# Kernel tuning notes

Hardware: AMD Instinct MI355X
Metric: run time of the kernel (lower is better)

## Reference

```python
import jax, jax.numpy as jnp
import numpy as np

B, NUM_FRAMES, NUM_PATCHES = 2, 16, 196
DIM, H, DH = 768, 12, 64
T = NUM_FRAMES * NUM_PATCHES  # 3136
EPS = 1e-5


def setup_inputs() -> dict:
    key = jax.random.key(0)
    ks = jax.random.split(key, 5)
    x = jax.random.normal(ks[0], (B, T, DIM), jnp.float32)
    context = jax.random.normal(ks[1], (B, T, DIM), jnp.float32)
    Wq = jax.random.normal(ks[2], (DIM, H * DH), jnp.float32) * 0.02
    Wkv = jax.random.normal(ks[3], (DIM, 2 * H * DH), jnp.float32) * 0.02
    Wo = jax.random.normal(ks[4], (H * DH, DIM), jnp.float32) * 0.02
    bo = jnp.zeros((DIM,), jnp.float32)
    gamma = jnp.ones((DIM,), jnp.float32)
    beta = jnp.zeros((DIM,), jnp.float32)
    # block-diagonal frame mask: patch i attends to patch j iff same frame
    frame_ids = jnp.arange(T) // NUM_PATCHES
    mask = frame_ids[:, None] == frame_ids[None, :]  # [T, T] bool
    return {"x": x, "context": context, "Wq": Wq, "Wkv": Wkv, "Wo": Wo,
            "bo": bo, "gamma": gamma, "beta": beta, "mask": mask}


def reference(x, context, Wq, Wkv, Wo, bo, gamma, beta, mask):
    # LayerNorm on queries only (torch LN: biased variance, eps=1e-5)
    mu = jnp.mean(x, axis=-1, keepdims=True)
    var = jnp.var(x, axis=-1, keepdims=True)
    xn = (x - mu) * jax.lax.rsqrt(var + EPS) * gamma + beta

    q = xn @ Wq                      # [B, T, H*DH]
    kv = context @ Wkv               # [B, T, 2*H*DH]
    k, v = jnp.split(kv, 2, axis=-1)

    def split_heads(t):
        return t.reshape(B, T, H, DH).transpose(0, 2, 1, 3)  # [B, H, T, DH]

    q, k, v = split_heads(q), split_heads(k), split_heads(v)

    scale = DH ** -0.5
    dots = jnp.einsum('bhnd,bhmd->bhnm', q, k) * scale      # [B, H, T, T]
    dots = jnp.where(mask, dots, -jnp.inf)
    attn = jax.nn.softmax(dots, axis=-1)                    # dropout p=0.0 -> identity
    out = jnp.einsum('bhnm,bhmd->bhnd', attn, v)            # [B, H, T, DH]
    out = out.transpose(0, 2, 1, 3).reshape(B, T, H * DH)
    return out @ Wo + bo
```

## Files before the change

kernel.cpp:

```cpp
#include <hip/hip_runtime.h>
#include <hip/hip_bf16.h>

#define NB 2
#define TT 3136
#define DIM 768
#define NH 12
#define NF 16
#define NP 196

typedef __attribute__((ext_vector_type(8))) short short8;
typedef __attribute__((ext_vector_type(4))) short s16x4;
typedef __attribute__((ext_vector_type(4))) float f32x4;
typedef unsigned int uint;

__device__ __forceinline__ float bf2f(short s) {
    return __uint_as_float(((uint)(unsigned short)s) << 16);
}
__device__ __forceinline__ short f2bs(float f) {
    __hip_bfloat16 h = __float2bfloat16(f);
    short s; __builtin_memcpy(&s, &h, 2); return s;
}
__device__ __forceinline__ uint pack2bf(float a, float b) {
    return (uint)(unsigned short)f2bs(a) | ((uint)(unsigned short)f2bs(b) << 16);
}
__device__ __forceinline__ void load16_lds(const void* g, void* l) {
    __builtin_amdgcn_global_load_lds(
        (const __attribute__((address_space(1))) unsigned int*)g,
        (__attribute__((address_space(3))) unsigned int*)l, 16, 0, 0);
}

__global__ __launch_bounds__(256)
void prep_all(const float* __restrict__ Wq, const float* __restrict__ Wkv,
              const float* __restrict__ Wo,
              __hip_bfloat16* __restrict__ WqT, __hip_bfloat16* __restrict__ WkvT,
              __hip_bfloat16* __restrict__ WoT,
              const float* __restrict__ ctx, __hip_bfloat16* __restrict__ cb,
              const float* __restrict__ x, const float* __restrict__ gamma,
              const float* __restrict__ beta, __hip_bfloat16* __restrict__ xn) {
    __shared__ float tile[32][33];
    int blk = blockIdx.x, tid = threadIdx.x;
    if (blk < 2304) {
        int bx = blk % 96, ky = blk / 96;
        const float* W; __hip_bfloat16* WT; int N, n0;
        if (bx < 24)      { W = Wq;  WT = WqT;  N = DIM;     n0 = bx * 32; }
        else if (bx < 72) { W = Wkv; WT = WkvT; N = 2 * DIM; n0 = (bx - 24) * 32; }
        else              { W = Wo;  WT = WoT;  N = DIM;     n0 = (bx - 72) * 32; }
        int k0 = ky * 32;
        int tx = tid & 31, ty = tid >> 5;
#pragma unroll
        for (int i = 0; i < 32; i += 8)
            tile[ty + i][tx] = W[(size_t)(k0 + ty + i) * N + (n0 + tx)];
        __syncthreads();
#pragma unroll
        for (int i = 0; i < 32; i += 8)
            WT[(size_t)(n0 + ty + i) * DIM + (k0 + tx)] = __float2bfloat16(tile[tx][ty + i]);
        return;
    }
    blk -= 2304;
    if (blk < 4704) {
        size_t i = (size_t)blk * 256 + tid;
        f32x4 f; __builtin_memcpy(&f, ctx + i * 4, 16);
        s16x4 s;
#pragma unroll
        for (int j = 0; j < 4; j++) s[j] = f2bs(f[j]);
        __builtin_memcpy((short*)cb + i * 4, &s, 8);
        return;
    }
    blk -= 4704;
    int wave = tid >> 6, lane = tid & 63;
    int row = blk * 4 + wave;
    const float* xr = x + (size_t)row * DIM;
    f32x4 v[3];
    float s = 0.f, ss = 0.f;
#pragma unroll
    for (int i = 0; i < 3; i++) {
        __builtin_memcpy(&v[i], xr + lane * 4 + i * 256, 16);
#pragma unroll
        for (int j = 0; j < 4; j++) { s += v[i][j]; ss += v[i][j] * v[i][j]; }
    }
#pragma unroll
    for (int off = 32; off; off >>= 1) {
        s += __shfl_xor(s, off);
        ss += __shfl_xor(ss, off);
    }
    float mu = s / DIM;
    float rs = rsqrtf(ss / DIM - mu * mu + 1e-5f);
#pragma unroll
    for (int i = 0; i < 3; i++) {
        int c = lane * 4 + i * 256;
        f32x4 g, bt;
        __builtin_memcpy(&g, gamma + c, 16);
        __builtin_memcpy(&bt, beta + c, 16);
        s16x4 o;
#pragma unroll
        for (int j = 0; j < 4; j++) o[j] = f2bs((v[i][j] - mu) * rs * g[j] + bt[j]);
        __builtin_memcpy((short*)xn + (size_t)row * DIM + c, &o, 8);
    }
}

__global__ __launch_bounds__(512, 1)
void gemm_qkv(const __hip_bfloat16* __restrict__ xn,
              const __hip_bfloat16* __restrict__ cb,
              const __hip_bfloat16* __restrict__ WqT,
              const __hip_bfloat16* __restrict__ WkvT,
              __hip_bfloat16* __restrict__ qbuf,
              __hip_bfloat16* __restrict__ kvbuf) {
    __shared__ short lds[2][2][2][8192];

    int orig = blockIdx.x;
    int xcd = orig & 7, pos = orig >> 3;
    int wgid = (xcd < 1 ? xcd * 29 : 29 + (xcd - 1) * 28) + pos;
    int mt = wgid / 9, nt = wgid - mt * 9;

    const __hip_bfloat16 *Abase, *Bbase; __hip_bfloat16* Cbase;
    int N, n0;
    if (nt < 3) { Abase = xn; Bbase = WqT;  Cbase = qbuf;  N = DIM;  n0 = nt * 256; }
    else        { Abase = cb; Bbase = WkvT; Cbase = kvbuf; N = 1536; n0 = (nt - 3) * 256; }
    int m0 = mt * 256;

    int tid = threadIdx.x, lane = tid & 63, wave = tid >> 6;
    int r = lane & 15, q = lane >> 4;
    int wm = wave >> 2, wn = wave & 3;
    f32x4 acc[8][4] = {};

    auto stageK = [&](int buf, int kt) {
        int k0 = kt * 64;
#pragma unroll
        for (int h = 0; h < 2; h++)
#pragma unroll
            for (int s = 0; s < 2; s++) {
                int idx = s * 512 + tid;
                int row = idx >> 3, cg = idx & 7;
                int w = (cg << 4) ^ ((row & 7) << 4);
                int grow = m0 + h * 128 + row;
                if (grow > TT * NB - 1) grow = TT * NB - 1;
                load16_lds((const char*)Abase + ((size_t)grow * DIM + k0) * 2 + w,
                           (char*)&lds[buf][0][h][0] + idx * 16);
            }
#pragma unroll
        for (int h = 0; h < 2; h++)
#pragma unroll
            for (int s = 0; s < 2; s++) {
                int idx = s * 512 + tid;
                int row = idx >> 3, cg = idx & 7;
                int w = (cg << 4) ^ ((row & 7) << 4);
                int grow = n0 + h * 128 + row;
                load16_lds((const char*)Bbase + ((size_t)grow * DIM + k0) * 2 + w,
                           (char*)&lds[buf][1][h][0] + idx * 16);
            }
    };

    auto read_frag = [&](const char* base, int frag, int ks) {
        short8 v;
        int row_ = frag * 16 + r;
        int byte_ = row_ * 128 + ((ks * 64 + q * 16) ^ ((r & 7) << 4));
        __builtin_memcpy(&v, base + byte_, 16);
        return v;
    };

    stageK(0, 0);
    asm volatile("s_waitcnt vmcnt(0)" ::: "memory");
    __builtin_amdgcn_s_barrier();

    for (int t = 0; t < 12; ++t) {
        int cur = t & 1;
        const char* Ah = (const char*)&lds[cur][0][wm][0];
        const char* Bh = (const char*)&lds[cur][1][wn >> 1][0];
        int bbase = (wn & 1) * 4;
        short8 breg[4][2];
#pragma unroll
        for (int p = 0; p < 4; p++) {
            short8 areg[2][2];
#pragma unroll
            for (int i = 0; i < 2; i++)
#pragma unroll
                for (int ks = 0; ks < 2; ks++)
                    areg[i][ks] = read_frag(Ah, p * 2 + i, ks);
            if (p == 0) {
#pragma unroll
                for (int n = 0; n < 4; n++)
#pragma unroll
                    for (int ks = 0; ks < 2; ks++)
                        breg[n][ks] = read_frag(Bh, bbase + n, ks);
                if (t < 11) stageK(cur ^ 1, t + 1);
            }
            __builtin_amdgcn_s_barrier();
            __builtin_amdgcn_s_setprio(1);
#pragma unroll
            for (int i = 0; i < 2; i++)
#pragma unroll
                for (int n = 0; n < 4; n++)
#pragma unroll
                    for (int ks = 0; ks < 2; ks++)
                        acc[p * 2 + i][n] = __builtin_amdgcn_mfma_f32_16x16x32_bf16(
                            areg[i][ks], breg[n][ks], acc[p * 2 + i][n], 0, 0, 0);
            __builtin_amdgcn_s_setprio(0);
            if (p == 3)
                asm volatile("s_waitcnt vmcnt(0)" ::: "memory");
            __builtin_amdgcn_s_barrier();
        }
    }

#pragma unroll
    for (int mf = 0; mf < 8; mf++)
#pragma unroll
        for (int n = 0; n < 4; n++)
#pragma unroll
            for (int rr = 0; rr < 4; rr++) {
                int row = m0 + wm * 128 + mf * 16 + q * 4 + rr;
                if (row < TT * NB) {
                    int col = n0 + wn * 64 + n * 16 + r;
                    Cbase[(size_t)row * N + col] = __float2bfloat16(acc[mf][n][rr]);
                }
            }
}

__global__ __launch_bounds__(256)
void gemm_o(const __hip_bfloat16* __restrict__ A,
            const __hip_bfloat16* __restrict__ BT,
            const float* __restrict__ bias,
            float* __restrict__ C) {
    __shared__ short sA[2][128 * 64];
    __shared__ short sB[2][128 * 64];
    int orig = blockIdx.x;
    int xcd = orig & 7, pos = orig >> 3;
    int wgid = (xcd < 6 ? xcd * 37 : 222 + (xcd - 6) * 36) + pos;
    int mt = wgid / 6, nt = wgid - mt * 6;
    int m0 = mt * 128, n0 = nt * 128;
    int tid = threadIdx.x, lane = tid & 63, wave = tid >> 6;
    int r = lane & 15, q = lane >> 4;
    int wm = (wave & 1) * 64, wn = (wave >> 1) * 64;
    f32x4 acc[4][4] = {};

    auto stage = [&](int buf, int k0) {
#pragma unroll
        for (int i = 0; i < 4; i++) {
            int c = i * 256 + tid;
            int row = c >> 3, cg = c & 7;
            load16_lds(A + (size_t)(m0 + row) * DIM + k0 + cg * 8, &sA[buf][c * 8]);
        }
#pragma unroll
        for (int i = 0; i < 4; i++) {
            int c = i * 256 + tid;
            int row = c >> 3, cg = c & 7;
            load16_lds(BT + (size_t)(n0 + row) * DIM + k0 + cg * 8, &sB[buf][c * 8]);
        }
    };
    auto compute = [&](int buf) {
#pragma unroll
        for (int ks = 0; ks < 2; ks++) {
            short8 af[4], bfv[4];
#pragma unroll
            for (int t = 0; t < 4; t++) {
                __builtin_memcpy(&af[t],  &sA[buf][(wm + t * 16 + r) * 64 + ks * 32 + q * 8], 16);
                __builtin_memcpy(&bfv[t], &sB[buf][(wn + t * 16 + r) * 64 + ks * 32 + q * 8], 16);
            }
            __builtin_amdgcn_s_setprio(1);
#pragma unroll
            for (int mi = 0; mi < 4; mi++)
#pragma unroll
                for (int ni = 0; ni < 4; ni++)
                    acc[mi][ni] = __builtin_amdgcn_mfma_f32_16x16x32_bf16(
                        af[mi], bfv[ni], acc[mi][ni], 0, 0, 0);
            __builtin_amdgcn_s_setprio(0);
        }
    };

    stage(0, 0);
    __syncthreads();
    int cur = 0;
#pragma unroll 2
    for (int t = 0; t < 11; ++t) {
        stage(cur ^ 1, (t + 1) * 64);
        compute(cur);
        __syncthreads();
        cur ^= 1;
    }
    compute(cur);

    float bv[4];
#pragma unroll
    for (int ni = 0; ni < 4; ni++) bv[ni] = bias[n0 + wn + ni * 16 + r];
#pragma unroll
    for (int mi = 0; mi < 4; mi++)
#pragma unroll
        for (int ni = 0; ni < 4; ni++)
#pragma unroll
            for (int rr = 0; rr < 4; rr++) {
                int row = m0 + wm + mi * 16 + q * 4 + rr;
                int col = n0 + wn + ni * 16 + r;
                C[(size_t)row * DIM + col] = acc[mi][ni][rr] + bv[ni];
            }
}

__global__ __launch_bounds__(448, 4)
void attn_kernel(__hip_bfloat16* qo,
                 const __hip_bfloat16* __restrict__ kvb) {
    __shared__ short sK[208 * 66];
    __shared__ short sVT[64 * 226];
    int blk = blockIdx.x;
    int f = blk % NF, h = (blk / NF) % NH, b = blk / (NF * NH);
    size_t tok0 = (size_t)b * TT + (size_t)f * NP;
    int tid = threadIdx.x, wave = tid >> 6, lane = tid & 63;
    int r = lane & 15, q = lane >> 4;

    short8 qf[2][2];
#pragma unroll
    for (int half = 0; half < 2; half++) {
        int qrow = half * 98 + wave * 16 + r;
        if (qrow >= NP) qrow = 0;
        const __hip_bfloat16* src = qo + (tok0 + qrow) * DIM + h * 64;
        __builtin_memcpy(&qf[half][0], src + q * 8, 16);
        __builtin_memcpy(&qf[half][1], src + 32 + q * 8, 16);
    }

    for (int e = tid; e < 1664; e += 448) {
        int row = e >> 3, cg = e & 7;
        short8 t = {0,0,0,0,0,0,0,0};
        if (row < NP)
            __builtin_memcpy(&t, kvb + (tok0 + row) * 1536 + h * 64 + cg * 8, 16);
        __builtin_memcpy(&sK[row * 66 + cg * 8], &t, 16);
    }
    for (int jj = 0; jj < 224; jj += 28) {
        int j = jj + (tid >> 4);
        int d = (tid & 15) * 4;
        s16x4 v = {0, 0, 0, 0};
        if (j < NP)
            __builtin_memcpy(&v, kvb + (tok0 + j) * 1536 + DIM + h * 64 + d, 8);
#pragma unroll
        for (int i = 0; i < 4; i++) sVT[(d + i) * 226 + j] = v[i];
    }
    __syncthreads();

#pragma unroll
    for (int half = 0; half < 2; half++) {
        int row0 = half * 98;

        f32x4 sacc[13];
#pragma unroll
        for (int jf = 0; jf < 13; jf++) {
            f32x4 a = {};
            short8 kf;
            __builtin_memcpy(&kf, &sK[(jf * 16 + r) * 66 + q * 8], 16);
            a = __builtin_amdgcn_mfma_f32_16x16x32_bf16(kf, qf[half][0], a, 0, 0, 0);
            __builtin_memcpy(&kf, &sK[(jf * 16 + r) * 66 + 32 + q * 8], 16);
            a = __builtin_amdgcn_mfma_f32_16x16x32_bf16(kf, qf[half][1], a, 0, 0, 0);
            sacc[jf] = a;
        }

        const float scale = 0.125f;
        float mx = -INFINITY;
#pragma unroll
        for (int jf = 0; jf < 13; jf++)
#pragma unroll
            for (int rg = 0; rg < 4; rg++) {
                bool valid = (jf < 12) | (q == 0);
                if (valid) mx = fmaxf(mx, sacc[jf][rg] * scale);
            }
        mx = fmaxf(mx, __shfl_xor(mx, 16));
        mx = fmaxf(mx, __shfl_xor(mx, 32));
        float ps = 0.f;
#pragma unroll
        for (int jf = 0; jf < 13; jf++)
#pragma unroll
            for (int rg = 0; rg < 4; rg++) {
                bool valid = (jf < 12) | (q == 0);
                float p = valid ? __expf(sacc[jf][rg] * scale - mx) : 0.f;
                sacc[jf][rg] = p;
                ps += p;
            }
        ps += __shfl_xor(ps, 16);
        ps += __shfl_xor(ps, 32);
        float inv = 1.f / ps;

        uint pk01[13], pk23[13];
#pragma unroll
        for (int jf = 0; jf < 13; jf++) {
            pk01[jf] = pack2bf(sacc[jf][0] * inv, sacc[jf][1] * inv);
            pk23[jf] = pack2bf(sacc[jf][2] * inv, sacc[jf][3] * inv);
        }
        int sl = (((2 * q) & 3) << 4) | r;
        int sh = (((2 * q + 1) & 3) << 4) | r;
        bool hiq = q >= 2;
        short8 pa[7];
#pragma unroll
        for (int c = 0; c < 7; c++) {
            uint a0 = (uint)__shfl((int)pk01[2 * c], sl, 64);
            uint a1 = (uint)__shfl((int)pk23[2 * c], sl, 64);
            uint a2 = (uint)__shfl((int)pk01[2 * c], sh, 64);
            uint a3 = (uint)__shfl((int)pk23[2 * c], sh, 64);
            uint b0 = 0, b1 = 0, b2 = 0, b3 = 0;
            if (c < 6) {
                b0 = (uint)__shfl((int)pk01[2 * c + 1], sl, 64);
                b1 = (uint)__shfl((int)pk23[2 * c + 1], sl, 64);
                b2 = (uint)__shfl((int)pk01[2 * c + 1], sh, 64);
                b3 = (uint)__shfl((int)pk23[2 * c + 1], sh, 64);
            }
            uint w[4] = { hiq ? b0 : a0, hiq ? b1 : a1, hiq ? b2 : a2, hiq ? b3 : a3 };
            __builtin_memcpy(&pa[c], w, 16);
        }

#pragma unroll
        for (int nt = 0; nt < 4; nt++) {
            f32x4 oacc = {};
#pragma unroll
            for (int kc = 0; kc < 7; kc++) {
                short8 bfv;
                __builtin_memcpy(&bfv, &sVT[(nt * 16 + r) * 226 + kc * 32 + q * 8], 16);
                oacc = __builtin_amdgcn_mfma_f32_16x16x32_bf16(pa[kc], bfv, oacc, 0, 0, 0);
            }
#pragma unroll
            for (int rg = 0; rg < 4; rg++) {
                int local = wave * 16 + q * 4 + rg;
                if (local < 98)
                    qo[(tok0 + row0 + local) * DIM + h * 64 + nt * 16 + r] =
                        __float2bfloat16(oacc[rg]);
            }
        }
    }
}

extern "C" void kernel_launch(void* const* d_in, const int* in_sizes, int n_in,
                              void* d_out, int out_size, void* d_ws, size_t ws_size,
                              hipStream_t stream) {
    const float* x     = (const float*)d_in[0];
    const float* ctx   = (const float*)d_in[1];
    const float* Wq    = (const float*)d_in[2];
    const float* Wkv   = (const float*)d_in[3];
    const float* Wo    = (const float*)d_in[4];
    const float* bo    = (const float*)d_in[5];
    const float* gamma = (const float*)d_in[6];
    const float* beta  = (const float*)d_in[7];

    char* ws = (char*)d_ws;
    __hip_bfloat16* cbuf  = (__hip_bfloat16*)(ws + 0);
    __hip_bfloat16* kvbuf = (__hip_bfloat16*)(ws + 9633792);
    __hip_bfloat16* qbuf  = (__hip_bfloat16*)(ws + 28901376);
    __hip_bfloat16* WqT   = (__hip_bfloat16*)(ws + 38535168);
    __hip_bfloat16* WkvT  = (__hip_bfloat16*)(ws + 39714816);
    __hip_bfloat16* WoT   = (__hip_bfloat16*)(ws + 42074112);
    __hip_bfloat16* xnbuf = (__hip_bfloat16*)d_out;
    float*          out   = (float*)d_out;

    prep_all<<<8576, 256, 0, stream>>>(Wq, Wkv, Wo, WqT, WkvT, WoT,
                                       ctx, cbuf, x, gamma, beta, xnbuf);
    gemm_qkv<<<225, 512, 0, stream>>>(xnbuf, cbuf, WqT, WkvT, qbuf, kvbuf);
    attn_kernel<<<NB * NH * NF, 448, 0, stream>>>(qbuf, kvbuf);
    gemm_o<<<294, 256, 0, stream>>>(qbuf, WoT, bo, out);
}
```

Baseline: 198.0 us.

## Switch QKV and output GEMMs to 4-stage K=32 LDS pipeline with XOR swizzle

Both projection GEMMs now stage K slices of 32 instead of 64 into a four-buffer LDS ring. Each stage issues three tiles ahead and waits with a partial vmcnt, so global loads overlap more MFMA work. Fragment reads use a new 4-way XOR swizzle to avoid LDS bank conflicts, and the QKV kernel's inner phased barrier loop is simplified to a single compute per stage. The trade-off is more barriers per K step and an epilogue that relies on an exact count of outstanding vmcnt loads.

Result: slower. 203.3 us (+2.6%).

```diff
diff --git a/kernel.cpp b/kernel.cpp
--- a/kernel.cpp
+++ b/kernel.cpp
@@ -105,7 +105,7 @@
               const __hip_bfloat16* __restrict__ WkvT,
               __hip_bfloat16* __restrict__ qbuf,
               __hip_bfloat16* __restrict__ kvbuf) {
-    __shared__ short lds[2][2][2][8192];
+    __shared__ short lds[4][2][8192];
 
     int orig = blockIdx.x;
     int xcd = orig & 7, pos = orig >> 3;
@@ -124,82 +124,65 @@
     f32x4 acc[8][4] = {};
 
     auto stageK = [&](int buf, int kt) {
-        int k0 = kt * 64;
-#pragma unroll
-        for (int h = 0; h < 2; h++)
-#pragma unroll
-            for (int s = 0; s < 2; s++) {
-                int idx = s * 512 + tid;
-                int row = idx >> 3, cg = idx & 7;
-                int w = (cg << 4) ^ ((row & 7) << 4);
-                int grow = m0 + h * 128 + row;
-                if (grow > TT * NB - 1) grow = TT * NB - 1;
-                load16_lds((const char*)Abase + ((size_t)grow * DIM + k0) * 2 + w,
-                           (char*)&lds[buf][0][h][0] + idx * 16);
-            }
-#pragma unroll
-        for (int h = 0; h < 2; h++)
-#pragma unroll
-            for (int s = 0; s < 2; s++) {
-                int idx = s * 512 + tid;
-                int row = idx >> 3, cg = idx & 7;
-                int w = (cg << 4) ^ ((row & 7) << 4);
-                int grow = n0 + h * 128 + row;
-                load16_lds((const char*)Bbase + ((size_t)grow * DIM + k0) * 2 + w,
-                           (char*)&lds[buf][1][h][0] + idx * 16);
-            }
-    };
-
-    auto read_frag = [&](const char* base, int frag, int ks) {
+        int k0 = kt * 32;
+#pragma unroll
+        for (int s = 0; s < 2; s++) {
+            int idx = s * 512 + tid;
+            int row = idx >> 2, cg = idx & 3;
+            int swz = (cg ^ (row & 3)) << 3;
+            int grow = m0 + row;
+            if (grow > TT * NB - 1) grow = TT * NB - 1;
+            load16_lds(Abase + (size_t)grow * DIM + k0 + swz, &lds[buf][0][idx * 8]);
+        }
+#pragma unroll
+        for (int s = 0; s < 2; s++) {
+            int idx = s * 512 + tid;
+            int row = idx >> 2, cg = idx & 3;
+            int swz = (cg ^ (row & 3)) << 3;
+            load16_lds(Bbase + (size_t)(n0 + row) * DIM + k0 + swz, &lds[buf][1][idx * 8]);
+        }
+    };
+
+    auto read_frag = [&](const short* base, int frag16row) {
         short8 v;
-        int row_ = frag * 16 + r;
-        int byte_ = row_ * 128 + ((ks * 64 + q * 16) ^ ((r & 7) << 4));
-        __builtin_memcpy(&v, base + byte_, 16);
+        int row_ = frag16row + r;
+        __builtin_memcpy(&v, base + row_ * 32 + ((q ^ (r & 3)) << 3), 16);
         return v;
     };
 
-    stageK(0, 0);
+    auto compute = [&](int cur) {
+        short8 af[8], bf[4];
+#pragma unroll
+        for (int m = 0; m < 8; m++) af[m] = read_frag(&lds[cur][0][0], wm * 128 + m * 16);
+#pragma unroll
+        for (int n = 0; n < 4; n++) bf[n] = read_frag(&lds[cur][1][0], wn * 64 + n * 16);
+        __builtin_amdgcn_s_setprio(1);
+#pragma unroll
+        for (int m = 0; m < 8; m++)
+#pragma unroll
+            for (int n = 0; n < 4; n++)
+                acc[m][n] = __builtin_amdgcn_mfma_f32_16x16x32_bf16(
+                    af[m], bf[n], acc[m][n], 0, 0, 0);
+        __builtin_amdgcn_s_setprio(0);
+    };
+
+    stageK(0, 0); stageK(1, 1); stageK(2, 2);
+    asm volatile("s_waitcnt vmcnt(8)" ::: "memory");
+    __builtin_amdgcn_s_barrier();
+
+    for (int t = 0; t < 21; ++t) {
+        stageK((t + 3) & 3, t + 3);
+        compute(t & 3);
+        asm volatile("s_waitcnt vmcnt(8)" ::: "memory");
+        __builtin_amdgcn_s_barrier();
+    }
+    compute(21 & 3);
+    asm volatile("s_waitcnt vmcnt(4)" ::: "memory");
+    __builtin_amdgcn_s_barrier();
+    compute(22 & 3);
     asm volatile("s_waitcnt vmcnt(0)" ::: "memory");
     __builtin_amdgcn_s_barrier();
-
-    for (int t = 0; t < 12; ++t) {
-        int cur = t & 1;
-        const char* Ah = (const char*)&lds[cur][0][wm][0];
-        const char* Bh = (const char*)&lds[cur][1][wn >> 1][0];
-        int bbase = (wn & 1) * 4;
-        short8 breg[4][2];
-#pragma unroll
-        for (int p = 0; p < 4; p++) {
-            short8 areg[2][2];
-#pragma unroll
-            for (int i = 0; i < 2; i++)
-#pragma unroll
-                for (int ks = 0; ks < 2; ks++)
-                    areg[i][ks] = read_frag(Ah, p * 2 + i, ks);
-            if (p == 0) {
-#pragma unroll
-                for (int n = 0; n < 4; n++)
-#pragma unroll
-                    for (int ks = 0; ks < 2; ks++)
-                        breg[n][ks] = read_frag(Bh, bbase + n, ks);
-                if (t < 11) stageK(cur ^ 1, t + 1);
-            }
-            __builtin_amdgcn_s_barrier();
-            __builtin_amdgcn_s_setprio(1);
-#pragma unroll
-            for (int i = 0; i < 2; i++)
-#pragma unroll
-                for (int n = 0; n < 4; n++)
-#pragma unroll
-                    for (int ks = 0; ks < 2; ks++)
-                        acc[p * 2 + i][n] = __builtin_amdgcn_mfma_f32_16x16x32_bf16(
-                            areg[i][ks], breg[n][ks], acc[p * 2 + i][n], 0, 0, 0);
-            __builtin_amdgcn_s_setprio(0);
-            if (p == 3)
-                asm volatile("s_waitcnt vmcnt(0)" ::: "memory");
-            __builtin_amdgcn_s_barrier();
-        }
-    }
+    compute(23 & 3);
 
 #pragma unroll
     for (int mf = 0; mf < 8; mf++)
@@ -220,8 +203,8 @@
             const __hip_bfloat16* __restrict__ BT,
             const float* __restrict__ bias,
             float* __restrict__ C) {
-    __shared__ short sA[2][128 * 64];
-    __shared__ short sB[2][128 * 64];
+    __shared__ short lds[4][2][4096];
+
     int orig = blockIdx.x;
     int xcd = orig & 7, pos = orig >> 3;
     int wgid = (xcd < 6 ? xcd * 37 : 222 + (xcd - 6) * 36) + pos;
@@ -232,51 +215,64 @@
     int wm = (wave & 1) * 64, wn = (wave >> 1) * 64;
     f32x4 acc[4][4] = {};
 
-    auto stage = [&](int buf, int k0) {
-#pragma unroll
-        for (int i = 0; i < 4; i++) {
-            int c = i * 256 + tid;
-            int row = c >> 3, cg = c & 7;
-            load16_lds(A + (size_t)(m0 + row) * DIM + k0 + cg * 8, &sA[buf][c * 8]);
-        }
-#pragma unroll
-        for (int i = 0; i < 4; i++) {
-            int c = i * 256 + tid;
-            int row = c >> 3, cg = c & 7;
-            load16_lds(BT + (size_t)(n0 + row) * DIM + k0 + cg * 8, &sB[buf][c * 8]);
-        }
-    };
-    auto compute = [&](int buf) {
-#pragma unroll
-        for (int ks = 0; ks < 2; ks++) {
-            short8 af[4], bfv[4];
-#pragma unroll
-            for (int t = 0; t < 4; t++) {
-                __builtin_memcpy(&af[t],  &sA[buf][(wm + t * 16 + r) * 64 + ks * 32 + q * 8], 16);
-                __builtin_memcpy(&bfv[t], &sB[buf][(wn + t * 16 + r) * 64 + ks * 32 + q * 8], 16);
-            }
-            __builtin_amdgcn_s_setprio(1);
-#pragma unroll
-            for (int mi = 0; mi < 4; mi++)
-#pragma unroll
-                for (int ni = 0; ni < 4; ni++)
-                    acc[mi][ni] = __builtin_amdgcn_mfma_f32_16x16x32_bf16(
-                        af[mi], bfv[ni], acc[mi][ni], 0, 0, 0);
-            __builtin_amdgcn_s_setprio(0);
-        }
-    };
-
-    stage(0, 0);
-    __syncthreads();
-    int cur = 0;
-#pragma unroll 2
-    for (int t = 0; t < 11; ++t) {
-        stage(cur ^ 1, (t + 1) * 64);
-        compute(cur);
-        __syncthreads();
-        cur ^= 1;
-    }
-    compute(cur);
+    auto stageK = [&](int buf, int kt) {
+        int k0 = kt * 32;
+#pragma unroll
+        for (int s = 0; s < 2; s++) {
+            int idx = s * 256 + tid;
+            int row = idx >> 2, cg = idx & 3;
+            int swz = (cg ^ (row & 3)) << 3;
+            load16_lds(A + (size_t)(m0 + row) * DIM + k0 + swz, &lds[buf][0][idx * 8]);
+        }
+#pragma unroll
+        for (int s = 0; s < 2; s++) {
+            int idx = s * 256 + tid;
+            int row = idx >> 2, cg = idx & 3;
+            int swz = (cg ^ (row & 3)) << 3;
+            load16_lds(BT + (size_t)(n0 + row) * DIM + k0 + swz, &lds[buf][1][idx * 8]);
+        }
+    };
+
+    auto read_frag = [&](const short* base, int frag16row) {
+        short8 v;
+        int row_ = frag16row + r;
+        __builtin_memcpy(&v, base + row_ * 32 + ((q ^ (r & 3)) << 3), 16);
+        return v;
+    };
+
+    auto compute = [&](int cur) {
+        short8 af[4], bf[4];
+#pragma unroll
+        for (int m = 0; m < 4; m++) af[m] = read_frag(&lds[cur][0][0], wm + m * 16);
+#pragma unroll
+        for (int n = 0; n < 4; n++) bf[n] = read_frag(&lds[cur][1][0], wn + n * 16);
+        __builtin_amdgcn_s_setprio(1);
+#pragma unroll
+        for (int m = 0; m < 4; m++)
+#pragma unroll
+            for (int n = 0; n < 4; n++)
+                acc[m][n] = __builtin_amdgcn_mfma_f32_16x16x32_bf16(
+                    af[m], bf[n], acc[m][n], 0, 0, 0);
+        __builtin_amdgcn_s_setprio(0);
+    };
+
+    stageK(0, 0); stageK(1, 1); stageK(2, 2);
+    asm volatile("s_waitcnt vmcnt(8)" ::: "memory");
+    __builtin_amdgcn_s_barrier();
+
+    for (int t = 0; t < 21; ++t) {
+        stageK((t + 3) & 3, t + 3);
+        compute(t & 3);
+        asm volatile("s_waitcnt vmcnt(8)" ::: "memory");
+        __builtin_amdgcn_s_barrier();
+    }
+    compute(21 & 3);
+    asm volatile("s_waitcnt vmcnt(4)" ::: "memory");
+    __builtin_amdgcn_s_barrier();
+    compute(22 & 3);
+    asm volatile("s_waitcnt vmcnt(0)" ::: "memory");
+    __builtin_amdgcn_s_barrier();
+    compute(23 & 3);
 
     float bv[4];
 #pragma unroll
```

## Fuse context fp32-to-bf16 conversion into QKV GEMM A-tile staging

Applied to the files above, without the earlier changes.

Drops the separate pass in prep_all that converted the fp32 context to a bf16 workspace buffer. KV tiles of the QKV GEMM now load fp32 context into registers, convert it to bf16 and write it to LDS with the same swizzle, while Q tiles keep using direct global-to-LDS loads. This removes one full write and reread of a large bf16 copy of the context. In exchange it reads twice as many bytes per A tile, adds register pressure, and puts an LDS write plus wait on the critical path before the barrier. Launch bounds are also raised to 2 blocks per CU.

Result: slower. 212.6 us (+7.4%).

```diff
diff --git a/kernel.cpp b/kernel.cpp
--- a/kernel.cpp
+++ b/kernel.cpp
@@ -34,7 +34,6 @@
               const float* __restrict__ Wo,
               __hip_bfloat16* __restrict__ WqT, __hip_bfloat16* __restrict__ WkvT,
               __hip_bfloat16* __restrict__ WoT,
-              const float* __restrict__ ctx, __hip_bfloat16* __restrict__ cb,
               const float* __restrict__ x, const float* __restrict__ gamma,
               const float* __restrict__ beta, __hip_bfloat16* __restrict__ xn) {
     __shared__ float tile[32][33];
@@ -57,16 +56,6 @@
         return;
     }
     blk -= 2304;
-    if (blk < 4704) {
-        size_t i = (size_t)blk * 256 + tid;
-        f32x4 f; __builtin_memcpy(&f, ctx + i * 4, 16);
-        s16x4 s;
-#pragma unroll
-        for (int j = 0; j < 4; j++) s[j] = f2bs(f[j]);
-        __builtin_memcpy((short*)cb + i * 4, &s, 8);
-        return;
-    }
-    blk -= 4704;
     int wave = tid >> 6, lane = tid & 63;
     int row = blk * 4 + wave;
     const float* xr = x + (size_t)row * DIM;
@@ -98,9 +87,9 @@
     }
 }
 
-__global__ __launch_bounds__(512, 1)
+__global__ __launch_bounds__(512, 2)
 void gemm_qkv(const __hip_bfloat16* __restrict__ xn,
-              const __hip_bfloat16* __restrict__ cb,
+              const float* __restrict__ ctxf,
               const __hip_bfloat16* __restrict__ WqT,
               const __hip_bfloat16* __restrict__ WkvT,
               __hip_bfloat16* __restrict__ qbuf,
@@ -112,18 +101,20 @@
     int wgid = (xcd < 1 ? xcd * 29 : 29 + (xcd - 1) * 28) + pos;
     int mt = wgid / 9, nt = wgid - mt * 9;
 
-    const __hip_bfloat16 *Abase, *Bbase; __hip_bfloat16* Cbase;
+    bool isKV = (nt >= 3);
+    const __hip_bfloat16* Bbase; __hip_bfloat16* Cbase;
     int N, n0;
-    if (nt < 3) { Abase = xn; Bbase = WqT;  Cbase = qbuf;  N = DIM;  n0 = nt * 256; }
-    else        { Abase = cb; Bbase = WkvT; Cbase = kvbuf; N = 1536; n0 = (nt - 3) * 256; }
+    if (!isKV) { Bbase = WqT;  Cbase = qbuf;  N = DIM;  n0 = nt * 256; }
+    else       { Bbase = WkvT; Cbase = kvbuf; N = 1536; n0 = (nt - 3) * 256; }
     int m0 = mt * 256;
 
     int tid = threadIdx.x, lane = tid & 63, wave = tid >> 6;
     int r = lane & 15, q = lane >> 4;
     int wm = wave >> 2, wn = wave & 3;
     f32x4 acc[8][4] = {};
-
-    auto stageK = [&](int buf, int kt) {
+    f32x4 rga[8];
+
+    auto stageB = [&](int buf, int kt) {
         int k0 = kt * 64;
 #pragma unroll
         for (int h = 0; h < 2; h++)
@@ -132,22 +123,47 @@
                 int idx = s * 512 + tid;
                 int row = idx >> 3, cg = idx & 7;
                 int w = (cg << 4) ^ ((row & 7) << 4);
-                int grow = m0 + h * 128 + row;
-                if (grow > TT * NB - 1) grow = TT * NB - 1;
-                load16_lds((const char*)Abase + ((size_t)grow * DIM + k0) * 2 + w,
-                           (char*)&lds[buf][0][h][0] + idx * 16);
-            }
+                load16_lds((const char*)Bbase + ((size_t)(n0 + h * 128 + row) * DIM + k0) * 2 + w,
+                           (char*)&lds[buf][1][h][0] + idx * 16);
+            }
+    };
+    auto stageA = [&](int buf, int kt) {
+        int k0 = kt * 64;
 #pragma unroll
         for (int h = 0; h < 2; h++)
 #pragma unroll
             for (int s = 0; s < 2; s++) {
                 int idx = s * 512 + tid;
                 int row = idx >> 3, cg = idx & 7;
-                int w = (cg << 4) ^ ((row & 7) << 4);
-                int grow = n0 + h * 128 + row;
-                load16_lds((const char*)Bbase + ((size_t)grow * DIM + k0) * 2 + w,
-                           (char*)&lds[buf][1][h][0] + idx * 16);
-            }
+                int off = (cg ^ (row & 7)) << 3;
+                int grow = m0 + h * 128 + row;
+                if (grow > TT * NB - 1) grow = TT * NB - 1;
+                if (isKV) {
+                    const float* src = ctxf + (size_t)grow * DIM + k0 + off;
+                    __builtin_memcpy(&rga[(h * 2 + s) * 2 + 0], src, 16);
+                    __builtin_memcpy(&rga[(h * 2 + s) * 2 + 1], src + 4, 16);
+                } else {
+                    load16_lds((const char*)xn + ((size_t)grow * DIM + k0) * 2 + (off << 1),
+                               (char*)&lds[buf][0][h][0] + idx * 16);
+                }
+            }
+    };
+    auto commitA = [&](int buf) {
+        if (!isKV) return;
+#pragma unroll
+        for (int h = 0; h < 2; h++)
+#pragma unroll
+            for (int s = 0; s < 2; s++) {
+                int idx = s * 512 + tid;
+                short8 o;
+#pragma unroll
+                for (int j = 0; j < 4; j++) {
+                    o[j]     = f2bs(rga[(h * 2 + s) * 2 + 0][j]);
+                    o[4 + j] = f2bs(rga[(h * 2 + s) * 2 + 1][j]);
+                }
+                __builtin_memcpy(&lds[buf][0][h][idx * 8], &o, 16);
+            }
+        asm volatile("s_waitcnt lgkmcnt(0)" ::: "memory");
     };
 
     auto read_frag = [&](const char* base, int frag, int ks) {
@@ -158,8 +174,9 @@
         return v;
     };
 
-    stageK(0, 0);
+    stageA(0, 0); stageB(0, 0);
     asm volatile("s_waitcnt vmcnt(0)" ::: "memory");
+    commitA(0);
     __builtin_amdgcn_s_barrier();
 
     for (int t = 0; t < 12; ++t) {
@@ -182,7 +199,7 @@
 #pragma unroll
                     for (int ks = 0; ks < 2; ks++)
                         breg[n][ks] = read_frag(Bh, bbase + n, ks);
-                if (t < 11) stageK(cur ^ 1, t + 1);
+                if (t < 11) { stageA(cur ^ 1, t + 1); stageB(cur ^ 1, t + 1); }
             }
             __builtin_amdgcn_s_barrier();
             __builtin_amdgcn_s_setprio(1);
@@ -195,8 +212,10 @@
                         acc[p * 2 + i][n] = __builtin_amdgcn_mfma_f32_16x16x32_bf16(
                             areg[i][ks], breg[n][ks], acc[p * 2 + i][n], 0, 0, 0);
             __builtin_amdgcn_s_setprio(0);
-            if (p == 3)
+            if (p == 3) {
                 asm volatile("s_waitcnt vmcnt(0)" ::: "memory");
+                if (t < 11) commitA(cur ^ 1);
+            }
             __builtin_amdgcn_s_barrier();
         }
     }
@@ -433,18 +452,17 @@
     const float* beta  = (const float*)d_in[7];
 
     char* ws = (char*)d_ws;
-    __hip_bfloat16* cbuf  = (__hip_bfloat16*)(ws + 0);
-    __hip_bfloat16* kvbuf = (__hip_bfloat16*)(ws + 9633792);
-    __hip_bfloat16* qbuf  = (__hip_bfloat16*)(ws + 28901376);
-    __hip_bfloat16* WqT   = (__hip_bfloat16*)(ws + 38535168);
-    __hip_bfloat16* WkvT  = (__hip_bfloat16*)(ws + 39714816);
-    __hip_bfloat16* WoT   = (__hip_bfloat16*)(ws + 42074112);
+    __hip_bfloat16* kvbuf = (__hip_bfloat16*)(ws + 0);
+    __hip_bfloat16* qbuf  = (__hip_bfloat16*)(ws + 19267584);
+    __hip_bfloat16* WqT   = (__hip_bfloat16*)(ws + 28901376);
+    __hip_bfloat16* WkvT  = (__hip_bfloat16*)(ws + 30081024);
+    __hip_bfloat16* WoT   = (__hip_bfloat16*)(ws + 32440320);
     __hip_bfloat16* xnbuf = (__hip_bfloat16*)d_out;
     float*          out   = (float*)d_out;
 
-    prep_all<<<8576, 256, 0, stream>>>(Wq, Wkv, Wo, WqT, WkvT, WoT,
-                                       ctx, cbuf, x, gamma, beta, xnbuf);
-    gemm_qkv<<<225, 512, 0, stream>>>(xnbuf, cbuf, WqT, WkvT, qbuf, kvbuf);
+    prep_all<<<3872, 256, 0, stream>>>(Wq, Wkv, Wo, WqT, WkvT, WoT,
+                                       x, gamma, beta, xnbuf);
+    gemm_qkv<<<225, 512, 0, stream>>>(xnbuf, ctx, WqT, WkvT, qbuf, kvbuf);
     attn_kernel<<<NB * NH * NF, 448, 0, stream>>>(qbuf, kvbuf);
     gemm_o<<<294, 256, 0, stream>>>(qbuf, WoT, bo, out);
 }
```

## Shrink QKV GEMM M-tile to 128 and use triple-buffered LDS pipeline

Applied to the files above, without the earlier changes.

The QKV projection GEMM now uses 128x256 output tiles instead of 256x256, which raises the grid from 225 to 441 workgroups and halves the accumulator registers per thread. The main loop is restructured into a 3-stage LDS ring that prefetches two K-steps ahead with a partial vmcnt wait, and it uses one barrier per K-step instead of eight. The aim is better CU occupancy and better latency hiding on the 256-CU part. The cost is more total global traffic for the B (weight) operand, and the row bound check is removed because 6272 is divisible by 128.

After: 205.7 us. 3.9% more time.

```diff
diff --git a/kernel.cpp b/kernel.cpp
--- a/kernel.cpp
+++ b/kernel.cpp
@@ -105,26 +105,34 @@
               const __hip_bfloat16* __restrict__ WkvT,
               __hip_bfloat16* __restrict__ qbuf,
               __hip_bfloat16* __restrict__ kvbuf) {
-    __shared__ short lds[2][2][2][8192];
+    __shared__ short lds[3][24576];
 
     int orig = blockIdx.x;
     int xcd = orig & 7, pos = orig >> 3;
-    int wgid = (xcd < 1 ? xcd * 29 : 29 + (xcd - 1) * 28) + pos;
+    int wgid = (xcd < 1 ? xcd * 56 : 56 + (xcd - 1) * 55) + pos;
     int mt = wgid / 9, nt = wgid - mt * 9;
 
     const __hip_bfloat16 *Abase, *Bbase; __hip_bfloat16* Cbase;
     int N, n0;
     if (nt < 3) { Abase = xn; Bbase = WqT;  Cbase = qbuf;  N = DIM;  n0 = nt * 256; }
     else        { Abase = cb; Bbase = WkvT; Cbase = kvbuf; N = 1536; n0 = (nt - 3) * 256; }
-    int m0 = mt * 256;
+    int m0 = mt * 128;
 
     int tid = threadIdx.x, lane = tid & 63, wave = tid >> 6;
     int r = lane & 15, q = lane >> 4;
     int wm = wave >> 2, wn = wave & 3;
-    f32x4 acc[8][4] = {};
-
-    auto stageK = [&](int buf, int kt) {
+    f32x4 acc[4][4] = {};
+
+    auto stageT = [&](int buf, int kt) {
         int k0 = kt * 64;
+#pragma unroll
+        for (int s = 0; s < 2; s++) {
+            int idx = s * 512 + tid;
+            int row = idx >> 3, cg = idx & 7;
+            int w = (cg << 4) ^ ((row & 7) << 4);
+            load16_lds((const char*)Abase + ((size_t)(m0 + row) * DIM + k0) * 2 + w,
+                       (char*)&lds[buf][0] + idx * 16);
+        }
 #pragma unroll
         for (int h = 0; h < 2; h++)
 #pragma unroll
@@ -132,86 +140,66 @@
                 int idx = s * 512 + tid;
                 int row = idx >> 3, cg = idx & 7;
                 int w = (cg << 4) ^ ((row & 7) << 4);
-                int grow = m0 + h * 128 + row;
-                if (grow > TT * NB - 1) grow = TT * NB - 1;
-                load16_lds((const char*)Abase + ((size_t)grow * DIM + k0) * 2 + w,
-                           (char*)&lds[buf][0][h][0] + idx * 16);
-            }
-#pragma unroll
-        for (int h = 0; h < 2; h++)
-#pragma unroll
-            for (int s = 0; s < 2; s++) {
-                int idx = s * 512 + tid;
-                int row = idx >> 3, cg = idx & 7;
-                int w = (cg << 4) ^ ((row & 7) << 4);
-                int grow = n0 + h * 128 + row;
-                load16_lds((const char*)Bbase + ((size_t)grow * DIM + k0) * 2 + w,
-                           (char*)&lds[buf][1][h][0] + idx * 16);
+                load16_lds((const char*)Bbase + ((size_t)(n0 + h * 128 + row) * DIM + k0) * 2 + w,
+                           (char*)&lds[buf][8192 + h * 8192] + idx * 16);
             }
     };
 
-    auto read_frag = [&](const char* base, int frag, int ks) {
+    auto read_frag = [&](const char* base, int frag_row, int ks) {
         short8 v;
-        int row_ = frag * 16 + r;
-        int byte_ = row_ * 128 + ((ks * 64 + q * 16) ^ ((r & 7) << 4));
+        int byte_ = frag_row * 128 + ((ks * 64 + q * 16) ^ ((r & 7) << 4));
         __builtin_memcpy(&v, base + byte_, 16);
         return v;
     };
 
-    stageK(0, 0);
-    asm volatile("s_waitcnt vmcnt(0)" ::: "memory");
+    auto compute = [&](int buf) {
+        const char* Ab = (const char*)&lds[buf][0];
+        const char* Bb = (const char*)&lds[buf][8192 + (wn >> 1) * 8192];
+        int brow0 = (wn & 1) * 64;
+        short8 af[4][2], bf[4][2];
+#pragma unroll
+        for (int m = 0; m < 4; m++)
+#pragma unroll
+            for (int ks = 0; ks < 2; ks++)
+                af[m][ks] = read_frag(Ab, wm * 64 + m * 16 + r, ks);
+#pragma unroll
+        for (int n = 0; n < 4; n++)
+#pragma unroll
+            for (int ks = 0; ks < 2; ks++)
+                bf[n][ks] = read_frag(Bb, brow0 + n * 16 + r, ks);
+        __builtin_amdgcn_s_setprio(1);
+#pragma unroll
+        for (int m = 0; m < 4; m++)
+#pragma unroll
+            for (int n = 0; n < 4; n++)
+#pragma unroll
+                for (int ks = 0; ks < 2; ks++)
+                    acc[m][n] = __builtin_amdgcn_mfma_f32_16x16x32_bf16(
+                        af[m][ks], bf[n][ks], acc[m][n], 0, 0, 0);
+        __builtin_amdgcn_s_setprio(0);
+    };
+
+    stageT(0, 0); stageT(1, 1);
+    asm volatile("s_waitcnt vmcnt(6)" ::: "memory");
     __builtin_amdgcn_s_barrier();
 
     for (int t = 0; t < 12; ++t) {
-        int cur = t & 1;
-        const char* Ah = (const char*)&lds[cur][0][wm][0];
-        const char* Bh = (const char*)&lds[cur][1][wn >> 1][0];
-        int bbase = (wn & 1) * 4;
-        short8 breg[4][2];
-#pragma unroll
-        for (int p = 0; p < 4; p++) {
-            short8 areg[2][2];
-#pragma unroll
-            for (int i = 0; i < 2; i++)
-#pragma unroll
-                for (int ks = 0; ks < 2; ks++)
-                    areg[i][ks] = read_frag(Ah, p * 2 + i, ks);
-            if (p == 0) {
-#pragma unroll
-                for (int n = 0; n < 4; n++)
-#pragma unroll
-                    for (int ks = 0; ks < 2; ks++)
-                        breg[n][ks] = read_frag(Bh, bbase + n, ks);
-                if (t < 11) stageK(cur ^ 1, t + 1);
-            }
-            __builtin_amdgcn_s_barrier();
-            __builtin_amdgcn_s_setprio(1);
-#pragma unroll
-            for (int i = 0; i < 2; i++)
-#pragma unroll
-                for (int n = 0; n < 4; n++)
-#pragma unroll
-                    for (int ks = 0; ks < 2; ks++)
-                        acc[p * 2 + i][n] = __builtin_amdgcn_mfma_f32_16x16x32_bf16(
-                            areg[i][ks], breg[n][ks], acc[p * 2 + i][n], 0, 0, 0);
-            __builtin_amdgcn_s_setprio(0);
-            if (p == 3)
-                asm volatile("s_waitcnt vmcnt(0)" ::: "memory");
-            __builtin_amdgcn_s_barrier();
-        }
-    }
-
-#pragma unroll
-    for (int mf = 0; mf < 8; mf++)
+        if (t < 10) stageT((t + 2) % 3, t + 2);
+        compute(t % 3);
+        if (t < 10)       asm volatile("s_waitcnt vmcnt(6)" ::: "memory");
+        else if (t == 10) asm volatile("s_waitcnt vmcnt(0)" ::: "memory");
+        if (t < 11) __builtin_amdgcn_s_barrier();
+    }
+
+#pragma unroll
+    for (int m = 0; m < 4; m++)
 #pragma unroll
         for (int n = 0; n < 4; n++)
 #pragma unroll
             for (int rr = 0; rr < 4; rr++) {
-                int row = m0 + wm * 128 + mf * 16 + q * 4 + rr;
-                if (row < TT * NB) {
-                    int col = n0 + wn * 64 + n * 16 + r;
-                    Cbase[(size_t)row * N + col] = __float2bfloat16(acc[mf][n][rr]);
-                }
+                int row = m0 + wm * 64 + m * 16 + q * 4 + rr;
+                int col = n0 + wn * 64 + n * 16 + r;
+                Cbase[(size_t)row * N + col] = __float2bfloat16(acc[m][n][rr]);
             }
 }
 
@@ -444,7 +432,7 @@
 
     prep_all<<<8576, 256, 0, stream>>>(Wq, Wkv, Wo, WqT, WkvT, WoT,
                                        ctx, cbuf, x, gamma, beta, xnbuf);
-    gemm_qkv<<<225, 512, 0, stream>>>(xnbuf, cbuf, WqT, WkvT, qbuf, kvbuf);
+    gemm_qkv<<<441, 512, 0, stream>>>(xnbuf, cbuf, WqT, WkvT, qbuf, kvbuf);
     attn_kernel<<<NB * NH * NF, 448, 0, stream>>>(qbuf, kvbuf);
     gemm_o<<<294, 256, 0, stream>>>(qbuf, WoT, bo, out);
 }
```
